# Optimization experiments

Hardware: AMD Instinct MI355X
Metric: run time of the kernel (lower is better)

## Reference

```python
import jax, jax.numpy as jnp
import numpy as np

EPS = 1e-8


def setup_inputs() -> dict:
    key = jax.random.key(0)
    kx, kw = jax.random.split(key)
    B, T, D_IN, D_OUT = 2, 2048, 4096, 16384
    x = jax.random.normal(kx, (B, T, D_IN), dtype=jnp.float32)
    # kaiming-uniform-ish scale for a (D_OUT, D_IN) linear weight
    bound = float(np.sqrt(6.0 / D_IN))
    weight = jax.random.uniform(kw, (D_OUT, D_IN), dtype=jnp.float32,
                                minval=-bound, maxval=bound)
    return {"x": x, "weight": weight}


def reference(x, weight):
    # --- ternary weight quantization (STE; value identical in train/eval) ---
    scale_w = jnp.mean(jnp.abs(weight))                       # scalar absmean
    w_q = jnp.clip(jnp.round(weight / (scale_w + EPS)), -1.0, 1.0) * scale_w
    w_quant = weight + jax.lax.stop_gradient(w_q - weight)    # STE

    # --- per-token INT8 activation quantization ---
    gamma = jnp.max(jnp.abs(x), axis=-1, keepdims=True)       # (B, T, 1)
    x_quant = jnp.clip(jnp.round(127.0 * x / (gamma + EPS)), -128.0, 127.0)
    scale_x = gamma / 127.0                                   # (B, T, 1)

    # --- GEMM + dequant epilogue ---
    out = jnp.einsum("btd,od->bto", x_quant, w_quant)         # (B, T, D_OUT)
    return out * scale_x
```

## Files before the change

### kernel.cpp

```cpp
#include <hip/hip_runtime.h>


#define M_ROWS 4096
#define K_DIM  4096
#define N_DIM  16384
#define W_ELEMS (N_DIM * K_DIM)
#define EPSF 1e-8f

using i32x4 = __attribute__((ext_vector_type(4))) int;

__global__ void k_abs_partial(const float4* __restrict__ w4,
                              double* __restrict__ part) {
    const int tid = threadIdx.x;
    int idx = blockIdx.x * 256 + tid;
    double s = 0.0;
    #pragma unroll 4
    for (int it = 0; it < 32; ++it) {
        float4 v = w4[idx + it * (2048 * 256)];
        s += (double)fabsf(v.x) + (double)fabsf(v.y)
           + (double)fabsf(v.z) + (double)fabsf(v.w);
    }
    __shared__ double red[256];
    red[tid] = s;
    __syncthreads();
    for (int o = 128; o > 0; o >>= 1) {
        if (tid < o) red[tid] += red[tid + o];
        __syncthreads();
    }
    if (tid == 0) part[blockIdx.x] = red[0];
}

__global__ void k_abs_final(const double* __restrict__ part,
                            float* __restrict__ scales) {
    const int tid = threadIdx.x;
    double s = 0.0;
    #pragma unroll
    for (int k = 0; k < 8; ++k) s += part[tid + k * 256];
    __shared__ double red[256];
    red[tid] = s;
    __syncthreads();
    for (int o = 128; o > 0; o >>= 1) {
        if (tid < o) red[tid] += red[tid + o];
        __syncthreads();
    }
    if (tid == 0) {
        float sw = (float)(red[0] / (double)W_ELEMS);
        scales[0] = sw;
        scales[1] = sw + EPSF;
    }
}

__global__ void k_wquant(const float4* __restrict__ w4,
                         const float* __restrict__ scales,
                         char4* __restrict__ wq4) {
    const float seps = scales[1];
    int idx = blockIdx.x * 256 + threadIdx.x;
    const int stride = 8192 * 256;
    #pragma unroll
    for (int it = 0; it < 8; ++it) {
        int i = idx + it * stride;
        float4 v = w4[i];
        char4 q;
        q.x = (signed char)(int)fminf(fmaxf(rintf(v.x / seps), -1.0f), 1.0f);
        q.y = (signed char)(int)fminf(fmaxf(rintf(v.y / seps), -1.0f), 1.0f);
        q.z = (signed char)(int)fminf(fmaxf(rintf(v.z / seps), -1.0f), 1.0f);
        q.w = (signed char)(int)fminf(fmaxf(rintf(v.w / seps), -1.0f), 1.0f);
        wq4[i] = q;
    }
}

__global__ void k_xquant(const float4* __restrict__ x4,
                         char4* __restrict__ xq4,
                         float* __restrict__ sx) {
    const int row = blockIdx.x, tid = threadIdx.x;
    const float4* xr = x4 + (size_t)row * (K_DIM / 4);
    float4 v[4];
    float m = 0.0f;
    #pragma unroll
    for (int j = 0; j < 4; ++j) {
        v[j] = xr[tid + j * 256];
        m = fmaxf(m, fmaxf(fmaxf(fabsf(v[j].x), fabsf(v[j].y)),
                           fmaxf(fabsf(v[j].z), fabsf(v[j].w))));
    }
    __shared__ float red[256];
    red[tid] = m;
    __syncthreads();
    for (int o = 128; o > 0; o >>= 1) {
        if (tid < o) red[tid] = fmaxf(red[tid], red[tid + o]);
        __syncthreads();
    }
    const float gamma = red[0];
    const float ge = gamma + EPSF;
    char4* out = xq4 + (size_t)row * (K_DIM / 4);
    #pragma unroll
    for (int j = 0; j < 4; ++j) {
        char4 q;
        q.x = (signed char)(int)fminf(fmaxf(rintf(127.0f * v[j].x / ge), -128.0f), 127.0f);
        q.y = (signed char)(int)fminf(fmaxf(rintf(127.0f * v[j].y / ge), -128.0f), 127.0f);
        q.z = (signed char)(int)fminf(fmaxf(rintf(127.0f * v[j].z / ge), -128.0f), 127.0f);
        q.w = (signed char)(int)fminf(fmaxf(rintf(127.0f * v[j].w / ge), -128.0f), 127.0f);
        out[tid + j * 256] = q;
    }
    if (tid == 0) sx[row] = gamma / 127.0f;
}

__device__ __forceinline__ void gload16(const signed char* g, signed char* l) {
    __builtin_amdgcn_global_load_lds(
        (const __attribute__((address_space(1))) void*)g,
        (__attribute__((address_space(3))) void*)l, 16, 0, 0);
}

#define BAR()   __builtin_amdgcn_s_barrier()
#define VM6()   asm volatile("s_waitcnt vmcnt(6)" ::: "memory")
#define PRIO1() __builtin_amdgcn_s_setprio(1)
#define PRIO0() __builtin_amdgcn_s_setprio(0)
#define SCHED0() __builtin_amdgcn_sched_barrier(0)

__global__ __launch_bounds__(512, 2)
void k_gemm8(const signed char* __restrict__ Aq,
             const signed char* __restrict__ Bq,
             const float* __restrict__ sx,
             const float* __restrict__ scales,
             float* __restrict__ C) {
    __shared__ __align__(16) signed char lds[131072];

    const int tid  = threadIdx.x;
    const int lane = tid & 63;
    const int wid  = tid >> 6;
    const int l15  = lane & 15;
    const int qg   = lane >> 4;
    const int swz  = l15 & 7;

    const int bid = blockIdx.x;
    const int wg  = (bid & 7) * 128 + (bid >> 3);
    const int gidx   = wg >> 9;
    const int within = wg & 511;
    const int pm = gidx * 8 + (within & 7);
    const int pn = within >> 3;

    const int wm = (wid >> 2) * 128;
    const int wn = (wid & 3) * 64;

    const int l3 = lane >> 3, l7 = lane & 7;
    const int lane_off = l3 * K_DIM + ((l7 ^ l3) << 4);
    const signed char* Asrc = Aq + (size_t)(pm * 256) * K_DIM + lane_off;
    const signed char* Bsrc = Bq + (size_t)(pn * 256) * K_DIM + lane_off;
    const int ar0 = wid * 8;
    const int br0 = (wid >> 2) * 64 + (wid & 3) * 8;

    auto stageA = [&](int buf, int mh, int kt) {
        const int r0 = mh * 64 + ar0;
        const signed char* s = Asrc + (size_t)r0 * K_DIM + kt * 128;
        signed char* d = lds + buf * 65536 + r0 * 128;
        gload16(s, d);
        gload16(s + (size_t)128 * K_DIM, d + 128 * 128);
    };
    auto stageB = [&](int buf, int nh, int kt) {
        const int r0 = nh * 32 + br0;
        const signed char* s = Bsrc + (size_t)r0 * K_DIM + kt * 128;
        signed char* d = lds + buf * 65536 + 32768 + r0 * 128;
        gload16(s, d);
        gload16(s + (size_t)128 * K_DIM, d + 128 * 128);
    };

    i32x4 acc[8][4];
    #pragma unroll
    for (int a = 0; a < 8; ++a)
        #pragma unroll
        for (int b = 0; b < 4; ++b)
            acc[a][b] = (i32x4){0, 0, 0, 0};

    i32x4 af[8], bf[4];
    auto ldA = [&](int buf, int mh) {
        const signed char* base = lds + buf * 65536;
        #pragma unroll
        for (int fm = 0; fm < 4; ++fm) {
            const int ro = (wm + mh * 64 + fm * 16 + l15) * 128;
            #pragma unroll
            for (int ks = 0; ks < 2; ++ks)
                af[fm * 2 + ks] = *(const i32x4*)(base + ro + (((ks * 4 + qg) ^ swz) << 4));
        }
    };
    auto ldB = [&](int buf, int nh) {
        const signed char* base = lds + buf * 65536 + 32768;
        #pragma unroll
        for (int fn = 0; fn < 2; ++fn) {
            const int ro = (wn + nh * 32 + fn * 16 + l15) * 128;
            #pragma unroll
            for (int ks = 0; ks < 2; ++ks)
                bf[fn * 2 + ks] = *(const i32x4*)(base + ro + (((ks * 4 + qg) ^ swz) << 4));
        }
    };
    auto mma = [&](int mh, int nh) {
        #pragma unroll
        for (int ks = 0; ks < 2; ++ks)
            #pragma unroll
            for (int fm = 0; fm < 4; ++fm)
                #pragma unroll
                for (int fn = 0; fn < 2; ++fn)
                    acc[mh * 4 + fm][nh * 2 + fn] = __builtin_amdgcn_mfma_i32_16x16x64_i8(
                        af[fm * 2 + ks], bf[fn * 2 + ks], acc[mh * 4 + fm][nh * 2 + fn], 0, 0, 0);
    };

    stageB(0, 0, 0); stageB(0, 1, 0); stageA(0, 0, 0); stageA(0, 1, 0);
    stageA(1, 0, 1); stageB(1, 1, 1); stageA(1, 1, 1);
    VM6();
    BAR();

    for (int t = 0; t < 16; ++t) {
        const int k1 = 2 * t + 1;
        const int k2 = (2 * t + 2) & 31;
        const int k3 = (2 * t + 3) & 31;

        ldA(0, 0); ldB(0, 0);
        stageB(1, 0, k1);
        BAR(); PRIO1(); mma(0, 0); PRIO0(); SCHED0();
        ldB(0, 1); SCHED0();
        BAR();
        stageA(0, 0, k2);
        BAR(); PRIO1(); mma(0, 1); PRIO0(); SCHED0();
        ldA(0, 1); SCHED0();
        BAR();
        stageB(0, 1, k2);
        BAR(); PRIO1(); mma(1, 1); PRIO0(); SCHED0();
        ldB(0, 0); SCHED0();
        BAR();
        stageA(0, 1, k2);
        BAR(); PRIO1(); mma(1, 0); PRIO0(); SCHED0();
        VM6();
        BAR();
        ldA(1, 0); ldB(1, 0);
        stageB(0, 0, k2);
        BAR(); PRIO1(); mma(0, 0); PRIO0(); SCHED0();
        ldB(1, 1); SCHED0();
        BAR();
        stageA(1, 0, k3);
        BAR(); PRIO1(); mma(0, 1); PRIO0(); SCHED0();
        ldA(1, 1); SCHED0();
        BAR();
        stageB(1, 1, k3);
        BAR(); PRIO1(); mma(1, 1); PRIO0(); SCHED0();
        ldB(1, 0); SCHED0();
        BAR();
        stageA(1, 1, k3);
        BAR(); PRIO1(); mma(1, 0); PRIO0(); SCHED0();
        VM6();
        BAR();
    }
    asm volatile("s_waitcnt vmcnt(0)" ::: "memory");

    const float sw = scales[0];
    const int gn0 = pn * 256 + wn + l15;
    const int rb  = (lane >> 4) * 4;
    #pragma unroll
    for (int mi = 0; mi < 8; ++mi) {
        const int rowoff = (mi >> 2) * 64 + (mi & 3) * 16;
        #pragma unroll
        for (int r = 0; r < 4; ++r) {
            const int gm = pm * 256 + wm + rowoff + rb + r;
            const float s = sx[gm] * sw;
            float* crow = C + (size_t)gm * N_DIM + gn0;
            #pragma unroll
            for (int ni = 0; ni < 4; ++ni)
                crow[(ni >> 1) * 32 + (ni & 1) * 16] = (float)acc[mi][ni][r] * s;
        }
    }
}

extern "C" void kernel_launch(void* const* d_in, const int* in_sizes, int n_in,
                              void* d_out, int out_size, void* d_ws, size_t ws_size,
                              hipStream_t stream) {
    const float* x = (const float*)d_in[0];
    const float* w = (const float*)d_in[1];
    float* out = (float*)d_out;
    char* ws = (char*)d_ws;

    float*  scales = (float*)(ws);
    double* part   = (double*)(ws + 1024);
    float*  sx     = (float*)(ws + 32 * 1024);
    signed char* xq = (signed char*)(ws + 64 * 1024);
    signed char* wq = xq + (size_t)M_ROWS * K_DIM;

    k_abs_partial<<<2048, 256, 0, stream>>>((const float4*)w, part);
    k_abs_final<<<1, 256, 0, stream>>>(part, scales);
    k_wquant<<<8192, 256, 0, stream>>>((const float4*)w, scales, (char4*)wq);
    k_xquant<<<M_ROWS, 256, 0, stream>>>((const float4*)x, (char4*)xq, sx);
    k_gemm8<<<(M_ROWS / 256) * (N_DIM / 256), 512, 0, stream>>>(xq, wq, sx, scales, out);
}
```

Measured before the change: 405.3 us.

## Regroup GEMM stage/MMA schedule to halve barriers per k-step

Restructures the int8 MFMA main loop so that two stage loads are issued together and two MMA quarters run back-to-back between barriers. This cuts the number of workgroup barriers per iteration from about sixteen to eight, and the vmcnt wait threshold drops from 6 to 4 to match the new issue pattern. The prologue defers one A-stage into the first iteration. The cost is less fine-grained interleaving of global-to-LDS loads with compute, plus possible LDS hazards if the buffer reuse ordering is now wrong.

```diff
diff --git a/kernel.cpp b/kernel.cpp
--- a/kernel.cpp
+++ b/kernel.cpp
@@ -111,7 +111,7 @@
 }
 
 #define BAR()   __builtin_amdgcn_s_barrier()
-#define VM6()   asm volatile("s_waitcnt vmcnt(6)" ::: "memory")
+#define VM4()   asm volatile("s_waitcnt vmcnt(4)" ::: "memory")
 #define PRIO1() __builtin_amdgcn_s_setprio(1)
 #define PRIO0() __builtin_amdgcn_s_setprio(0)
 #define SCHED0() __builtin_amdgcn_sched_barrier(0)
@@ -203,8 +203,8 @@
     };
 
     stageB(0, 0, 0); stageB(0, 1, 0); stageA(0, 0, 0); stageA(0, 1, 0);
-    stageA(1, 0, 1); stageB(1, 1, 1); stageA(1, 1, 1);
-    VM6();
+    stageA(1, 0, 1); stageB(1, 1, 1);
+    VM4();
     BAR();
 
     for (int t = 0; t < 16; ++t) {
@@ -213,38 +213,34 @@
         const int k3 = (2 * t + 3) & 31;
 
         ldA(0, 0); ldB(0, 0);
-        stageB(1, 0, k1);
-        BAR(); PRIO1(); mma(0, 0); PRIO0(); SCHED0();
+        stageB(1, 0, k1); stageA(1, 1, k1);
+        BAR();
+        PRIO1(); mma(0, 0); PRIO0(); SCHED0();
         ldB(0, 1); SCHED0();
-        BAR();
-        stageA(0, 0, k2);
-        BAR(); PRIO1(); mma(0, 1); PRIO0(); SCHED0();
-        ldA(0, 1); SCHED0();
-        BAR();
-        stageB(0, 1, k2);
-        BAR(); PRIO1(); mma(1, 1); PRIO0(); SCHED0();
+        PRIO1(); mma(0, 1); PRIO0(); SCHED0();
+        BAR();
+        ldA(0, 1);
+        stageA(0, 0, k2); stageB(0, 1, k2);
+        BAR();
+        PRIO1(); mma(1, 1); PRIO0(); SCHED0();
         ldB(0, 0); SCHED0();
-        BAR();
-        stageA(0, 1, k2);
-        BAR(); PRIO1(); mma(1, 0); PRIO0(); SCHED0();
-        VM6();
+        PRIO1(); mma(1, 0); PRIO0(); SCHED0();
+        VM4();
         BAR();
         ldA(1, 0); ldB(1, 0);
-        stageB(0, 0, k2);
-        BAR(); PRIO1(); mma(0, 0); PRIO0(); SCHED0();
+        stageA(0, 1, k2); stageB(0, 0, k2);
+        BAR();
+        PRIO1(); mma(0, 0); PRIO0(); SCHED0();
         ldB(1, 1); SCHED0();
-        BAR();
-        stageA(1, 0, k3);
-        BAR(); PRIO1(); mma(0, 1); PRIO0(); SCHED0();
-        ldA(1, 1); SCHED0();
-        BAR();
-        stageB(1, 1, k3);
-        BAR(); PRIO1(); mma(1, 1); PRIO0(); SCHED0();
+        PRIO1(); mma(0, 1); PRIO0(); SCHED0();
+        BAR();
+        ldA(1, 1);
+        stageA(1, 0, k3); stageB(1, 1, k3);
+        BAR();
+        PRIO1(); mma(1, 1); PRIO0(); SCHED0();
         ldB(1, 0); SCHED0();
-        BAR();
-        stageA(1, 1, k3);
-        BAR(); PRIO1(); mma(1, 0); PRIO0(); SCHED0();
-        VM6();
+        PRIO1(); mma(1, 0); PRIO0(); SCHED0();
+        VM4();
         BAR();
     }
     asm volatile("s_waitcnt vmcnt(0)" ::: "memory");
```

Measured after the change: 407.4 us. No clear change (+0.5%).
